# Optimization experiments

Measured on AMD Instinct MI355X. Metric: run time of the kernel, lower is better.

## Reference

```python
import jax, jax.numpy as jnp
import numpy as np

N_CLASSES = 91

def setup_inputs() -> dict:
    key = jax.random.key(0)
    k1, k2 = jax.random.split(key)
    B, H, W = 32, 1024, 1024
    inputs = jax.random.randint(k1, (B, H, W), 0, N_CLASSES, dtype=jnp.int32)
    targets = jax.random.randint(k2, (B, H, W), 0, N_CLASSES, dtype=jnp.int32)
    smooth = jnp.ones((1,), dtype=jnp.float32)  # original default smooth=1
    return {"inputs": inputs, "targets": targets, "smooth": smooth}

def reference(inputs, targets, smooth):
    # Single-pass histogram formulation of the original 91-iteration loop.
    B = inputs.shape[0]
    x = inputs.reshape(B, -1)   # [B, N] int labels
    t = targets.reshape(B, -1)  # [B, N]
    rows = jnp.arange(B)[:, None]
    # per-class counts: cnt_x[b,c] = #pixels with x==c (== a.sum per class)
    cnt_x = jnp.zeros((B, N_CLASSES), jnp.float32).at[rows, x].add(1.0)
    cnt_t = jnp.zeros((B, N_CLASSES), jnp.float32).at[rows, t].add(1.0)
    # intersection[b,c] = #pixels with x==t==c; route mismatches to a dump bin
    match = jnp.where(x == t, x, N_CLASSES)
    inter = jnp.zeros((B, N_CLASSES + 1), jnp.float32).at[rows, match].add(1.0)[:, :N_CLASSES]
    union = cnt_x + cnt_t - inter  # total - intersection
    s = smooth[0]
    iou = (inter + s) / (union + s)  # [B, C]
    return iou.mean(axis=1)          # sum_IoU / n_classes, shape [B]
```

## Files before the change

kernel.cpp:

```cpp
#include <hip/hip_runtime.h>

#define NC 91
#define NB 32
#define HW (1024 * 1024)

#define THREADS 256
#define PPT 64
#define PIX_PER_BLOCK (THREADS * PPT)
#define CHUNKS (HW / PIX_PER_BLOCK)
#define NPAIR (NC * NC)
#define NWORD ((NPAIR + 1) / 2)


__global__ __launch_bounds__(256, 8) void hist_kernel(const int* __restrict__ x,
                                                      const int* __restrict__ t,
                                                      int* __restrict__ g_cx,
                                                      int* __restrict__ g_ct,
                                                      int* __restrict__ g_in) {
    __shared__ int s_pair[NWORD];

    const int tid = threadIdx.x;
    for (int j = tid; j < NWORD; j += THREADS) s_pair[j] = 0;
    __syncthreads();

    const int b = blockIdx.y;
    const long base = (long)b * HW + (long)blockIdx.x * PIX_PER_BLOCK;
    const int4* __restrict__ x4 = (const int4*)(x + base);
    const int4* __restrict__ t4 = (const int4*)(t + base);

    const int n = PPT / 4;
    int4 xv0 = x4[tid],           tv0 = t4[tid];
    int4 xv1 = x4[THREADS + tid], tv1 = t4[THREADS + tid];

    for (int i = 0; i < n; ++i) {
        const int pf = (i + 2 < n) ? (i + 2) : (n - 1);
        int4 xn = x4[pf * THREADS + tid];
        int4 tn = t4[pf * THREADS + tid];

        const int b0 = xv0.x * NC + tv0.x;
        const int b1 = xv0.y * NC + tv0.y;
        const int b2 = xv0.z * NC + tv0.z;
        const int b3 = xv0.w * NC + tv0.w;
        atomicAdd(&s_pair[b0 >> 1], 1 << ((b0 & 1) << 4));
        atomicAdd(&s_pair[b1 >> 1], 1 << ((b1 & 1) << 4));
        atomicAdd(&s_pair[b2 >> 1], 1 << ((b2 & 1) << 4));
        atomicAdd(&s_pair[b3 >> 1], 1 << ((b3 & 1) << 4));

        xv0 = xv1; tv0 = tv1;
        xv1 = xn;  tv1 = tn;
    }
    __syncthreads();

    if (tid < NC) {
        int ct = 0;
        for (int xx = 0; xx < NC; ++xx) {
            const int bin = xx * NC + tid;
            ct += (s_pair[bin >> 1] >> ((bin & 1) << 4)) & 0xffff;
        }
        if (ct) atomicAdd(&g_ct[b * NC + tid], ct);
        const int dg = s_pair[tid * 46] & 0xffff;
        if (dg) atomicAdd(&g_in[b * NC + tid], dg);
    }
    else if (tid >= 128 && tid < 128 + NC) {
        const int c = tid - 128;
        int cx = 0;
        for (int tt = 0; tt < NC; ++tt) {
            const int bin = c * NC + tt;
            cx += (s_pair[bin >> 1] >> ((bin & 1) << 4)) & 0xffff;
        }
        if (cx) atomicAdd(&g_cx[b * NC + c], cx);
    }
}

__global__ __launch_bounds__(64) void finalize_kernel(const int* __restrict__ g_cx,
                                                      const int* __restrict__ g_ct,
                                                      const int* __restrict__ g_in,
                                                      const float* __restrict__ smooth,
                                                      float* __restrict__ out) {
    const int b = blockIdx.x;
    const int lane = threadIdx.x;
    const float s = smooth[0];
    float acc = 0.0f;
    for (int c = lane; c < NC; c += 64) {
        const float in = (float)g_in[b * NC + c];
        const float un = (float)(g_cx[b * NC + c] + g_ct[b * NC + c]) - in;
        acc += (in + s) / (un + s);
    }
#pragma unroll
    for (int off = 32; off > 0; off >>= 1)
        acc += __shfl_down(acc, off, 64);
    if (lane == 0) out[b] = acc / (float)NC;
}

extern "C" void kernel_launch(void* const* d_in, const int* in_sizes, int n_in,
                              void* d_out, int out_size, void* d_ws, size_t ws_size,
                              hipStream_t stream) {
    const int* x = (const int*)d_in[0];
    const int* t = (const int*)d_in[1];
    const float* smooth = (const float*)d_in[2];
    float* out = (float*)d_out;

    int* g_cx = (int*)d_ws;
    int* g_ct = g_cx + NB * NC;
    int* g_in = g_ct + NB * NC;

    hipMemsetAsync(d_ws, 0, 3 * NB * NC * sizeof(int), stream);

    dim3 grid(CHUNKS, NB);
    hist_kernel<<<grid, THREADS, 0, stream>>>(x, t, g_cx, g_ct, g_in);
    finalize_kernel<<<NB, 64, 0, stream>>>(g_cx, g_ct, g_in, smooth, out);
}
```

Baseline: 284.3 us.

## Stage input tiles through LDS with async global_load_lds double buffering

Replaces the register-level prefetch of input and target labels with direct global-to-LDS DMA loads (global_load_lds) into a double-buffered staging area, so the next chunk loads while the current chunk is histogrammed with LDS atomics. The aim is to keep memory traffic in flight without holding prefetched data in registers. In exchange each block uses about 32KB more LDS, which lowers occupancy, and adds a block-wide barrier per chunk. The occupancy hint in launch_bounds is also dropped.

```diff
diff --git a/kernel.cpp b/kernel.cpp
--- a/kernel.cpp
+++ b/kernel.cpp
@@ -5,51 +5,75 @@
 #define HW (1024 * 1024)
 
 #define THREADS 256
-#define PPT 64
-#define PIX_PER_BLOCK (THREADS * PPT)
-#define CHUNKS (HW / PIX_PER_BLOCK)
+#define PIX_PER_BLOCK 16384
+#define GRID_X (HW / PIX_PER_BLOCK)
+#define CPX 2048
+#define NCHUNK (PIX_PER_BLOCK / CPX)
 #define NPAIR (NC * NC)
 #define NWORD ((NPAIR + 1) / 2)
 
 
-__global__ __launch_bounds__(256, 8) void hist_kernel(const int* __restrict__ x,
-                                                      const int* __restrict__ t,
-                                                      int* __restrict__ g_cx,
-                                                      int* __restrict__ g_ct,
-                                                      int* __restrict__ g_in) {
+typedef __attribute__((address_space(3))) void lds_t;
+typedef __attribute__((address_space(1))) const void gm_t;
+
+__device__ __forceinline__ void dma16(const int* g, int* l) {
+    __builtin_amdgcn_global_load_lds((gm_t*)g, (lds_t*)l, 16, 0, 0);
+}
+
+__global__ __launch_bounds__(256) void hist_kernel(const int* __restrict__ x,
+                                                   const int* __restrict__ t,
+                                                   int* __restrict__ g_cx,
+                                                   int* __restrict__ g_ct,
+                                                   int* __restrict__ g_in) {
     __shared__ int s_pair[NWORD];
+    __shared__ int s_stage[2][2][CPX];
 
     const int tid = threadIdx.x;
+    const int lane = tid & 63;
+    const int wid = tid >> 6;
+
     for (int j = tid; j < NWORD; j += THREADS) s_pair[j] = 0;
-    __syncthreads();
 
     const int b = blockIdx.y;
     const long base = (long)b * HW + (long)blockIdx.x * PIX_PER_BLOCK;
-    const int4* __restrict__ x4 = (const int4*)(x + base);
-    const int4* __restrict__ t4 = (const int4*)(t + base);
+    const int* __restrict__ xg = x + base;
+    const int* __restrict__ tg = t + base;
 
-    const int n = PPT / 4;
-    int4 xv0 = x4[tid],           tv0 = t4[tid];
-    int4 xv1 = x4[THREADS + tid], tv1 = t4[THREADS + tid];
+#define ISSUE(c, bf)                                                      \
+    {                                                                     \
+        _Pragma("unroll")                                                 \
+        for (int k = 0; k < 2; ++k) {                                     \
+            const int j = wid * 2 + k;                                    \
+            const int off = (c) * CPX + j * 256 + lane * 4;               \
+            dma16(xg + off, &s_stage[bf][0][j * 256]);                    \
+            dma16(tg + off, &s_stage[bf][1][j * 256]);                    \
+        }                                                                 \
+    }
 
-    for (int i = 0; i < n; ++i) {
-        const int pf = (i + 2 < n) ? (i + 2) : (n - 1);
-        int4 xn = x4[pf * THREADS + tid];
-        int4 tn = t4[pf * THREADS + tid];
+    ISSUE(0, 0)
+    __syncthreads();
 
-        const int b0 = xv0.x * NC + tv0.x;
-        const int b1 = xv0.y * NC + tv0.y;
-        const int b2 = xv0.z * NC + tv0.z;
-        const int b3 = xv0.w * NC + tv0.w;
-        atomicAdd(&s_pair[b0 >> 1], 1 << ((b0 & 1) << 4));
-        atomicAdd(&s_pair[b1 >> 1], 1 << ((b1 & 1) << 4));
-        atomicAdd(&s_pair[b2 >> 1], 1 << ((b2 & 1) << 4));
-        atomicAdd(&s_pair[b3 >> 1], 1 << ((b3 & 1) << 4));
+    for (int c = 0; c < NCHUNK; ++c) {
+        const int bf = c & 1;
+        if (c + 1 < NCHUNK) ISSUE(c + 1, bf ^ 1)
 
-        xv0 = xv1; tv0 = tv1;
-        xv1 = xn;  tv1 = tn;
+        const int4* __restrict__ xs = (const int4*)s_stage[bf][0];
+        const int4* __restrict__ ts = (const int4*)s_stage[bf][1];
+#pragma unroll
+        for (int r = 0; r < 2; ++r) {
+            const int4 xv = xs[r * 256 + tid];
+            const int4 tv = ts[r * 256 + tid];
+            const int b0 = xv.x * NC + tv.x;
+            const int b1 = xv.y * NC + tv.y;
+            const int b2 = xv.z * NC + tv.z;
+            const int b3 = xv.w * NC + tv.w;
+            atomicAdd(&s_pair[b0 >> 1], 1 << ((b0 & 1) << 4));
+            atomicAdd(&s_pair[b1 >> 1], 1 << ((b1 & 1) << 4));
+            atomicAdd(&s_pair[b2 >> 1], 1 << ((b2 & 1) << 4));
+            atomicAdd(&s_pair[b3 >> 1], 1 << ((b3 & 1) << 4));
+        }
+        __syncthreads();
     }
-    __syncthreads();
 
     if (tid < NC) {
         int ct = 0;
@@ -60,8 +84,7 @@
         if (ct) atomicAdd(&g_ct[b * NC + tid], ct);
         const int dg = s_pair[tid * 46] & 0xffff;
         if (dg) atomicAdd(&g_in[b * NC + tid], dg);
-    }
-    else if (tid >= 128 && tid < 128 + NC) {
+    } else if (tid >= 128 && tid < 128 + NC) {
         const int c = tid - 128;
         int cx = 0;
         for (int tt = 0; tt < NC; ++tt) {
@@ -70,6 +93,7 @@
         }
         if (cx) atomicAdd(&g_cx[b * NC + c], cx);
     }
+#undef ISSUE
 }
 
 __global__ __launch_bounds__(64) void finalize_kernel(const int* __restrict__ g_cx,
@@ -106,7 +130,7 @@
 
     hipMemsetAsync(d_ws, 0, 3 * NB * NC * sizeof(int), stream);
 
-    dim3 grid(CHUNKS, NB);
+    dim3 grid(GRID_X, NB);
     hist_kernel<<<grid, THREADS, 0, stream>>>(x, t, g_cx, g_ct, g_in);
     finalize_kernel<<<NB, 64, 0, stream>>>(g_cx, g_ct, g_in, smooth, out);
 }
```

New measurement: 284.8 us. No clear change (+0.2%).
